# Kernel optimization log

Hardware: AMD Instinct MI355X
Metric: run time of the kernel (lower is better)

The kernel has to match this reference:

```python
import jax, jax.numpy as jnp
import numpy as np

NUM_CLASSES = 20
NUM_ANCHORS = 3
BBOX_ATTRS = 5 + NUM_CLASSES
IMG_H = IMG_W = 416
IN_H = IN_W = 52
CONF_THRES = 0.5
NMS_THRES = 0.4
TOP_K = 2048


def setup_inputs() -> dict:
    key = jax.random.key(0)
    k1, _ = jax.random.split(key)
    inp = jax.random.normal(k1, (16, NUM_ANCHORS * BBOX_ATTRS, IN_H, IN_W), dtype=jnp.float32)
    anchors = jnp.array([[116.0, 90.0], [156.0, 198.0], [373.0, 326.0]], dtype=jnp.float32)
    return {"input": inp, "anchors": anchors}


def decode(inp, anchors):
    """YOLOv3 head decode (YOLOv3Loss.forward with targets=None).
    inp: [B, A*(5+C), H, W] -> output: [B, A*H*W, 5+C] with (cx, cy, w, h, conf, cls...)."""
    bs = inp.shape[0]
    stride_h = IMG_H / IN_H
    stride_w = IMG_W / IN_W
    scaled_anchors = anchors / jnp.array([stride_w, stride_h], dtype=inp.dtype)  # [A, 2]
    # [B, A, H, W, 5+C]
    pred = inp.reshape(bs, NUM_ANCHORS, BBOX_ATTRS, IN_H, IN_W).transpose(0, 1, 3, 4, 2)
    x = jax.nn.sigmoid(pred[..., 0])
    y = jax.nn.sigmoid(pred[..., 1])
    w = pred[..., 2]
    h = pred[..., 3]
    conf = jax.nn.sigmoid(pred[..., 4])
    pred_cls = jax.nn.sigmoid(pred[..., 5:])
    grid_x = jnp.arange(IN_W, dtype=inp.dtype)[None, None, None, :]
    grid_y = jnp.arange(IN_H, dtype=inp.dtype)[None, None, :, None]
    anchor_w = scaled_anchors[:, 0][None, :, None, None]
    anchor_h = scaled_anchors[:, 1][None, :, None, None]
    bx = (x + grid_x) * stride_w
    by = (y + grid_y) * stride_h
    bw = jnp.exp(w) * anchor_w * stride_w
    bh = jnp.exp(h) * anchor_h * stride_h
    boxes = jnp.stack([bx, by, bw, bh], axis=-1).reshape(bs, -1, 4)
    output = jnp.concatenate(
        [boxes, conf.reshape(bs, -1, 1), pred_cls.reshape(bs, -1, NUM_CLASSES)], axis=-1
    )
    return output


def _nms_one(corners, conf, cls_pred):
    """Greedy class-aware NMS over TOP_K conf-sorted candidates.
    corners: [K,4] x1y1x2y2, conf: [K] desc-sorted, cls_pred: [K] int32.
    Returns keep mask [K] bool."""
    x1, y1, x2, y2 = corners[:, 0], corners[:, 1], corners[:, 2], corners[:, 3]
    area = (x2 - x1 + 1.0) * (y2 - y1 + 1.0)
    ix1 = jnp.maximum(x1[:, None], x1[None, :])
    iy1 = jnp.maximum(y1[:, None], y1[None, :])
    ix2 = jnp.minimum(x2[:, None], x2[None, :])
    iy2 = jnp.minimum(y2[:, None], y2[None, :])
    inter = jnp.clip(ix2 - ix1 + 1.0, 0.0) * jnp.clip(iy2 - iy1 + 1.0, 0.0)
    iou = inter / (area[:, None] + area[None, :] - inter + 1e-16)
    # suppress j if kept i (earlier, higher conf, same class) overlaps >= thres
    cond = (iou >= NMS_THRES) & (cls_pred[:, None] == cls_pred[None, :])
    valid = conf >= CONF_THRES
    K = conf.shape[0]
    idx = jnp.arange(K)

    def body(i, carry):
        keep, supp = carry
        ki = valid[i] & (~supp[i])
        keep = keep.at[i].set(ki)
        supp = supp | (cond[i] & (idx > i) & ki)
        return keep, supp

    keep, _ = jax.lax.fori_loop(0, K, body, (jnp.zeros(K, bool), jnp.zeros(K, bool)))
    return keep


def reference(input, anchors):
    output = decode(input, anchors)  # [B, N, 5+C]
    conf = output[..., 4]
    # top-K candidates by objectness (desc order == conf sort in original NMS)
    top_conf, top_idx = jax.lax.top_k(conf, TOP_K)  # [B, K]
    boxes = output[..., :4]
    cx, cy, w, h = boxes[..., 0], boxes[..., 1], boxes[..., 2], boxes[..., 3]
    corners = jnp.stack([cx - w / 2, cy - h / 2, cx + w / 2, cy + h / 2], axis=-1)
    corners_s = jnp.take_along_axis(corners, top_idx[..., None], axis=1)  # [B, K, 4]
    cls_pred = jnp.argmax(output[..., 5:], axis=-1).astype(jnp.int32)  # [B, N]
    cls_s = jnp.take_along_axis(cls_pred, top_idx, axis=1)  # [B, K]
    keep = jax.vmap(_nms_one)(corners_s, top_conf, cls_s)  # [B, K] bool
    return output, top_idx, keep
```

## Files before the change

### kernel.cpp

```cpp
#include <hip/hip_runtime.h>

#pragma clang fp contract(off)

#define B 16
#define A 3
#define HGT 52
#define WID 52
#define HW 2704
#define NCAND 8112
#define CATTR 25
#define TOPK 2048
#define NWORD 64
#define CH 256
#define NCHUNK (TOPK / CH)
#define GPC (CH / 32)
#define CHP 260
#define EPT 8

typedef unsigned int uint32;
typedef unsigned long long u64;

__global__ __launch_bounds__(256) void decode_kernel(const float* __restrict__ inp,
                                                     const float* __restrict__ anchors,
                                                     float* __restrict__ out,
                                                     float* __restrict__ cws,
                                                     float* __restrict__ pk) {
    __shared__ float sm[256 * CATTR];
    int tid = threadIdx.x;
    int t = blockIdx.x * 256 + tid;
    int b  = t / NCAND;
    int n  = t - b * NCAND;
    int a  = n / HW;
    int hw = n - a * HW;
    int gy = hw / WID;
    int gx = hw - gy * WID;
    const float* ip = inp + ((size_t)(b * (A * CATTR) + a * CATTR)) * HW + hw;
    float* sp = sm + tid * CATTR;

    float p0 = ip[0 * HW], p1 = ip[1 * HW], p2 = ip[2 * HW], p3 = ip[3 * HW], p4 = ip[4 * HW];
    float sx = 1.0f / (1.0f + expf(-p0));
    float sy = 1.0f / (1.0f + expf(-p1));
    float bx = (sx + (float)gx) * 8.0f;
    float by = (sy + (float)gy) * 8.0f;
    float bw = expf(p2) * anchors[a * 2 + 0];
    float bh = expf(p3) * anchors[a * 2 + 1];
    float cf = 1.0f / (1.0f + expf(-p4));
    sp[0] = bx; sp[1] = by; sp[2] = bw; sp[3] = bh; sp[4] = cf;
    cws[t] = cf;

    float best = -1.0f; int bc = 0;
#pragma unroll
    for (int c = 0; c < 20; ++c) {
        float v = ip[(5 + c) * HW];
        float s = 1.0f / (1.0f + expf(-v));
        sp[5 + c] = s;
        if (s > best) { best = s; bc = c; }
    }

    float hw_ = bw * 0.5f, hh_ = bh * 0.5f;
    float x1 = bx - hw_, y1 = by - hh_, x2 = bx + hw_, y2 = by + hh_;
    float area = ((x2 - x1) + 1.0f) * ((y2 - y1) + 1.0f);
    float4* pk4 = (float4*)(pk + (size_t)t * 8);
    pk4[0] = make_float4(x1, y1, x2, y2);
    pk4[1] = make_float4(area, (float)bc, (cf >= 0.5f) ? 1.0f : 0.0f, 0.0f);

    __syncthreads();
    const float4* sm4 = (const float4*)sm;
    float4* o4 = (float4*)(out + (size_t)blockIdx.x * 256 * CATTR);
#pragma unroll
    for (int k = 0; k < 6; ++k) o4[k * 256 + tid] = sm4[k * 256 + tid];
    if (tid < 64) o4[1536 + tid] = sm4[1536 + tid];
}

__device__ __forceinline__ void cexd(u64& a, u64& b, bool up) {
    if ((a > b) == up) { u64 tmp = a; a = b; b = tmp; }
}

__device__ __forceinline__ u64 sel(u64 k, u64 o, bool kmin) {
    return kmin ? (k < o ? k : o) : (k > o ? k : o);
}

__device__ __forceinline__ void bitonic_merge_2048(u64 key[EPT], u64* mb, int t) {
    for (unsigned j = 1024; j >= 8; j >>= 1) {
        unsigned m = j >> 3;
        bool kmin = ((t & m) == 0);
        if (m >= 64) {
            __syncthreads();
#pragma unroll
            for (int e = 0; e < EPT; ++e) mb[e * 256 + t] = key[e];
            __syncthreads();
            int pt = t ^ (int)m;
#pragma unroll
            for (int e = 0; e < EPT; ++e) key[e] = sel(key[e], mb[e * 256 + pt], kmin);
        } else {
#pragma unroll
            for (int e = 0; e < EPT; ++e) {
                u64 o = __shfl_xor(key[e], (int)m);
                key[e] = sel(key[e], o, kmin);
            }
        }
    }
    cexd(key[0], key[4], true); cexd(key[1], key[5], true);
    cexd(key[2], key[6], true); cexd(key[3], key[7], true);
    cexd(key[0], key[2], true); cexd(key[1], key[3], true);
    cexd(key[4], key[6], true); cexd(key[5], key[7], true);
    cexd(key[0], key[1], true); cexd(key[2], key[3], true);
    cexd(key[4], key[5], true); cexd(key[6], key[7], true);
}

__global__ __launch_bounds__(256) void sort1_kernel(const float* __restrict__ conf,
                                                    u64* __restrict__ runs) {
    __shared__ u64 mb[2048];
    int blk = blockIdx.x;
    int b = blk >> 2, c = blk & 3;
    int t = threadIdx.x;
    int base = t * EPT;
    int gbase = c * 2048 + base;
    const float* cp = conf + b * NCAND;

    u64 key[EPT];
    if (gbase + EPT <= NCAND) {
        const float4* cp4 = (const float4*)(cp + gbase);
        float4 c0 = cp4[0], c1 = cp4[1];
        float cf[EPT] = {c0.x, c0.y, c0.z, c0.w, c1.x, c1.y, c1.z, c1.w};
#pragma unroll
        for (int e = 0; e < EPT; ++e) {
            unsigned bits = __float_as_uint(cf[e]) | 0x80000000u;
            key[e] = ((u64)(~bits) << 32) | (unsigned)(gbase + e);
        }
    } else {
#pragma unroll
        for (int e = 0; e < EPT; ++e) {
            int idx = gbase + e;
            if (idx < NCAND) {
                unsigned bits = __float_as_uint(cp[idx]) | 0x80000000u;
                key[e] = ((u64)(~bits) << 32) | (unsigned)idx;
            } else key[e] = ~0ull;
        }
    }

    cexd(key[0], key[1], true); cexd(key[2], key[3], false);
    cexd(key[4], key[5], true); cexd(key[6], key[7], false);

    cexd(key[0], key[2], true);  cexd(key[1], key[3], true);
    cexd(key[4], key[6], false); cexd(key[5], key[7], false);
    cexd(key[0], key[1], true);  cexd(key[2], key[3], true);
    cexd(key[4], key[5], false); cexd(key[6], key[7], false);

    bool up8 = ((t & 1) == 0);
    cexd(key[0], key[4], up8); cexd(key[1], key[5], up8);
    cexd(key[2], key[6], up8); cexd(key[3], key[7], up8);
    cexd(key[0], key[2], up8); cexd(key[1], key[3], up8);
    cexd(key[4], key[6], up8); cexd(key[5], key[7], up8);
    cexd(key[0], key[1], up8); cexd(key[2], key[3], up8);
    cexd(key[4], key[5], up8); cexd(key[6], key[7], up8);

    for (unsigned k = 16; k <= 2048; k <<= 1) {
        bool up = (((unsigned)base & k) == 0);
        for (unsigned j = k >> 1; j >= 8; j >>= 1) {
            unsigned m = j >> 3;
            bool kmin = (up == ((t & m) == 0));
            if (m >= 64) {
                __syncthreads();
#pragma unroll
                for (int e = 0; e < EPT; ++e) mb[e * 256 + t] = key[e];
                __syncthreads();
                int pt = t ^ (int)m;
#pragma unroll
                for (int e = 0; e < EPT; ++e) key[e] = sel(key[e], mb[e * 256 + pt], kmin);
            } else {
#pragma unroll
                for (int e = 0; e < EPT; ++e) {
                    u64 o = __shfl_xor(key[e], (int)m);
                    key[e] = sel(key[e], o, kmin);
                }
            }
        }
        cexd(key[0], key[4], up); cexd(key[1], key[5], up);
        cexd(key[2], key[6], up); cexd(key[3], key[7], up);
        cexd(key[0], key[2], up); cexd(key[1], key[3], up);
        cexd(key[4], key[6], up); cexd(key[5], key[7], up);
        cexd(key[0], key[1], up); cexd(key[2], key[3], up);
        cexd(key[4], key[5], up); cexd(key[6], key[7], up);
    }

    u64* R = runs + ((size_t)b * 4 + c) * 2048;
#pragma unroll
    for (int e = 0; e < EPT; ++e) R[base + e] = key[e];
}

__global__ __launch_bounds__(256) void sort23_kernel(const u64* __restrict__ runs,
                                                     float* __restrict__ topf) {
    __shared__ u64 mb[2048];
    int b = blockIdx.x;
    int t = threadIdx.x;
    int base = t * EPT;
    const u64* R0 = runs + (size_t)b * 4 * 2048;

    u64 ka[EPT], kb[EPT];
#pragma unroll
    for (int e = 0; e < EPT; ++e) {
        u64 a = R0[base + e];
        u64 o = R0[2048 + 2047 - (base + e)];
        ka[e] = a < o ? a : o;
    }
    bitonic_merge_2048(ka, mb, t);
#pragma unroll
    for (int e = 0; e < EPT; ++e) {
        u64 a = R0[2 * 2048 + base + e];
        u64 o = R0[3 * 2048 + 2047 - (base + e)];
        kb[e] = a < o ? a : o;
    }
    bitonic_merge_2048(kb, mb, t);
    __syncthreads();
#pragma unroll
    for (int e = 0; e < EPT; ++e) mb[base + e] = kb[e];
    __syncthreads();
#pragma unroll
    for (int e = 0; e < EPT; ++e) {
        u64 o = mb[2047 - (base + e)];
        ka[e] = ka[e] < o ? ka[e] : o;
    }
    bitonic_merge_2048(ka, mb, t);

#pragma unroll
    for (int e = 0; e < EPT; ++e)
        topf[(size_t)b * TOPK + base + e] = (float)(unsigned)(ka[e] & 0xFFFFFFFFu);
}

__global__ __launch_bounds__(256) void geo_kernel(const float* __restrict__ pk,
                                                  const float* __restrict__ topf,
                                                  float* __restrict__ gx1,
                                                  float* __restrict__ gy1,
                                                  float* __restrict__ gx2,
                                                  float* __restrict__ gy2,
                                                  float* __restrict__ gar,
                                                  uint32* __restrict__ gcv,
                                                  uint32* __restrict__ vwords) {
    int t = blockIdx.x * 256 + threadIdx.x;
    int b = t >> 11;
    int idx = (int)topf[t];
    const float4* p4 = (const float4*)(pk + ((size_t)b * NCAND + idx) * 8);
    float4 g0 = p4[0], g1 = p4[1];
    gx1[t] = g0.x; gy1[t] = g0.y; gx2[t] = g0.z; gy2[t] = g0.w;
    gar[t] = g1.x;
    gcv[t] = (uint32)g1.y;
    bool valid = (g1.z != 0.0f);
    unsigned long long bal = __ballot(valid);
    if ((t & 63) == 0) {
        vwords[(t >> 5) + 0] = (uint32)bal;
        vwords[(t >> 5) + 1] = (uint32)(bal >> 32);
    }
}

#define KMID (13421772.5 / 33554432.0)
__global__ __launch_bounds__(1024) void build_kernel(const float* __restrict__ gx1,
                                                     const float* __restrict__ gy1,
                                                     const float* __restrict__ gx2,
                                                     const float* __restrict__ gy2,
                                                     const float* __restrict__ gar,
                                                     const uint32* __restrict__ gcv,
                                                     uint32* __restrict__ rowmask) {
    __shared__ float  x1s[TOPK], y1s[TOPK], x2s[TOPK], y2s[TOPK];
    __shared__ uint32 clss[TOPK];
    int bt   = blockIdx.y;
    int pr   = blockIdx.x;
    int tid  = threadIdx.x;
    int lane = tid & 63;
    int wv   = tid >> 6;
    int base = bt * TOPK;
    uint32* rmT = rowmask + (size_t)base * NWORD;

    for (int j = tid; j < TOPK; j += 1024) {
        int g = base + j;
        x1s[j] = gx1[g]; y1s[j] = gy1[g]; x2s[j] = gx2[g]; y2s[j] = gy2[g];
        clss[j] = gcv[g] & 0xffu;
    }
    __syncthreads();

    int r  = (wv >> 3) ? (31 - pr) : pr;
    int i0 = r * 64 + (wv & 7) * 8;

    float rx1[8], ry1[8], rx2[8], ry2[8], rar[8];
    uint32 rcl[8];
#pragma unroll
    for (int k = 0; k < 8; ++k) {
        rx1[k] = x1s[i0 + k]; ry1[k] = y1s[i0 + k];
        rx2[k] = x2s[i0 + k]; ry2[k] = y2s[i0 + k];
        rar[k] = ((rx2[k] - rx1[k]) + 1.0f) * ((ry2[k] - ry1[k]) + 1.0f);
        rcl[k] = clss[i0 + k];
    }

    int j0 = r * 64 + lane;
    float cx1 = x1s[j0], cy1 = y1s[j0], cx2 = x2s[j0], cy2 = y2s[j0];
    uint32 cc = clss[j0];

    for (int cg = r; cg < 32; ++cg) {
        float nx1 = 0.f, ny1 = 0.f, nx2 = 0.f, ny2 = 0.f; uint32 nc = 0;
        if (cg + 1 < 32) {
            int nj = (cg + 1) * 64 + lane;
            nx1 = x1s[nj]; ny1 = y1s[nj]; nx2 = x2s[nj]; ny2 = y2s[nj];
            nc = clss[nj];
        }
        float car = ((cx2 - cx1) + 1.0f) * ((cy2 - cy1) + 1.0f);
        u64 bal[8];
#pragma unroll
        for (int k = 0; k < 8; ++k) {
            float ix1 = fmaxf(rx1[k], cx1);
            float iy1 = fmaxf(ry1[k], cy1);
            float ix2 = fminf(rx2[k], cx2);
            float iy2 = fminf(ry2[k], cy2);
            float iw = fmaxf((ix2 - ix1) + 1.0f, 0.0f);
            float ih = fmaxf((iy2 - iy1) + 1.0f, 0.0f);
            float inter = iw * ih;
            float denom = ((rar[k] + car) - inter) + 1e-16f;
            bool cond = ((double)inter > KMID * (double)denom) && (cc == rcl[k]);
            bal[k] = __ballot(cond);
        }
        u64 v = bal[0];
#pragma unroll
        for (int k = 1; k < 8; ++k) if ((lane & 7) == k) v = bal[k];
        uint32 w32 = (lane & 8) ? (uint32)(v >> 32) : (uint32)v;
        int gi = i0 + (lane & 7);
        int wd = 2 * cg + ((lane >> 3) & 1);
        if (wd == (gi >> 5)) w32 &= ~((2u << (gi & 31)) - 1u);
        if (lane < 16) rmT[(size_t)wd * TOPK + gi] = w32;
        cx1 = nx1; cy1 = ny1; cx2 = nx2; cy2 = ny2; cc = nc;
    }
}

__device__ __forceinline__ void copy_chunk_dma(const uint32* __restrict__ rmT,
                                               uint32* dstL, int c, int wvm1, int lane) {
    int wmin = 8 * c;
    for (int w = wmin + wvm1; w < 64; w += 15) {
        const uint32* gp = rmT + (size_t)w * TOPK + c * CH + lane * 4;
        uint32* lp = dstL + w * CHP;
        __builtin_amdgcn_global_load_lds((const __attribute__((address_space(1))) void*)gp,
                                         (__attribute__((address_space(3))) void*)lp,
                                         16, 0, 0);
    }
}

__global__ __launch_bounds__(1024) void scan_kernel(const uint32* __restrict__ rowmask,
                                                    const uint32* __restrict__ vwords,
                                                    float* __restrict__ keepf) {
    __shared__ uint32 buf[2][64 * CHP];
    int bt  = blockIdx.x;
    int tid = threadIdx.x;
    int wv  = tid >> 6;
    int l   = tid & 63;
    const uint32* rmT = rowmask + (size_t)bt * TOPK * NWORD;

    uint32 supp = 0, keepw = 0;
    if (wv == 0) supp = ~vwords[bt * 64 + l];

    if (wv > 0) copy_chunk_dma(rmT, buf[0], 0, wv - 1, l);
    __syncthreads();

    for (int c = 0; c < NCHUNK; ++c) {
        if (wv > 0) {
            if (c + 1 < NCHUNK) copy_chunk_dma(rmT, buf[(c + 1) & 1], c + 1, wv - 1, l);
        } else {
            const uint32* bp = buf[c & 1];
            uint4 sq[8];
            {
                int g0 = c * GPC;
                const uint4* sp = (const uint4*)(bp + g0 * CHP);
#pragma unroll
                for (int q = 0; q < 8; ++q) sq[q] = sp[q];
            }
            for (int gl = 0; gl < GPC; ++gl) {
                int g = c * GPC + gl;
                uint4 rwq[8];
                const uint4* rp = (const uint4*)(bp + l * CHP + gl * 32);
#pragma unroll
                for (int q = 0; q < 8; ++q) rwq[q] = rp[q];
                uint32 cur = __builtin_amdgcn_readlane(supp, g);
#pragma unroll
                for (int q = 0; q < 8; ++q) {
                    uint32 s0 = sq[q].x, s1 = sq[q].y, s2 = sq[q].z, s3 = sq[q].w;
                    int k = q * 4;
                    cur |= s0 & ((((cur >> (k + 0)) & 1u)) - 1u);
                    cur |= s1 & ((((cur >> (k + 1)) & 1u)) - 1u);
                    cur |= s2 & ((((cur >> (k + 2)) & 1u)) - 1u);
                    cur |= s3 & ((((cur >> (k + 3)) & 1u)) - 1u);
                }
                uint32 keep = ~cur;
                if (l == g) keepw = keep;
                if (gl + 1 < GPC) {
                    const uint4* sp = (const uint4*)(bp + (g + 1) * CHP + (gl + 1) * 32);
#pragma unroll
                    for (int q = 0; q < 8; ++q) sq[q] = sp[q];
                }
                uint32 upd = 0;
#pragma unroll
                for (int q = 0; q < 8; ++q) {
                    int k = q * 4;
                    upd |= rwq[q].x & (uint32)(((int)(keep << (31 - (k + 0)))) >> 31);
                    upd |= rwq[q].y & (uint32)(((int)(keep << (31 - (k + 1)))) >> 31);
                    upd |= rwq[q].z & (uint32)(((int)(keep << (31 - (k + 2)))) >> 31);
                    upd |= rwq[q].w & (uint32)(((int)(keep << (31 - (k + 3)))) >> 31);
                }
                supp |= upd;
            }
        }
        __syncthreads();
    }

    if (wv == 0) {
#pragma unroll
        for (int k = 0; k < 32; ++k)
            keepf[bt * TOPK + l * 32 + k] = (float)((keepw >> k) & 1u);
    }
}

extern "C" void kernel_launch(void* const* d_in, const int* in_sizes, int n_in,
                              void* d_out, int out_size, void* d_ws, size_t ws_size,
                              hipStream_t stream) {
    const float* inp     = (const float*)d_in[0];
    const float* anchors = (const float*)d_in[1];
    float* out   = (float*)d_out;
    float* topf  = out  + (size_t)B * NCAND * CATTR;
    float* keepf = topf + (size_t)B * TOPK;

    float*  cws = (float*)d_ws;
    float*  pk  = cws + B * NCAND;
    float*  gx1 = pk  + (size_t)B * NCAND * 8;
    float*  gy1 = gx1 + B * TOPK;
    float*  gx2 = gy1 + B * TOPK;
    float*  gy2 = gx2 + B * TOPK;
    float*  gar = gy2 + B * TOPK;
    uint32* gcv = (uint32*)(gar + B * TOPK);
    uint32* rowmask = gcv + B * TOPK;
    uint32* vwords  = rowmask + (size_t)B * TOPK * NWORD;
    u64* runs = (u64*)rowmask;

    decode_kernel<<<(B * NCAND) / 256, 256, 0, stream>>>(inp, anchors, out, cws, pk);
    sort1_kernel<<<B * 4, 256, 0, stream>>>(cws, runs);
    sort23_kernel<<<B, 256, 0, stream>>>(runs, topf);
    geo_kernel<<<(B * TOPK) / 256, 256, 0, stream>>>(pk, topf, gx1, gy1, gx2, gy2, gar, gcv, vwords);
    build_kernel<<<dim3(16, B), 1024, 0, stream>>>(gx1, gy1, gx2, gy2, gar, gcv, rowmask);
    scan_kernel<<<B, 1024, 0, stream>>>(rowmask, vwords, keepf);
}
```

Baseline: 175.6 us.

## Replace single-block bitonic top-K merge with parallel merge-path rank kernels

```diff
diff --git a/kernel.cpp b/kernel.cpp
--- a/kernel.cpp
+++ b/kernel.cpp
@@ -80,34 +80,6 @@
     return kmin ? (k < o ? k : o) : (k > o ? k : o);
 }
 
-__device__ __forceinline__ void bitonic_merge_2048(u64 key[EPT], u64* mb, int t) {
-    for (unsigned j = 1024; j >= 8; j >>= 1) {
-        unsigned m = j >> 3;
-        bool kmin = ((t & m) == 0);
-        if (m >= 64) {
-            __syncthreads();
-#pragma unroll
-            for (int e = 0; e < EPT; ++e) mb[e * 256 + t] = key[e];
-            __syncthreads();
-            int pt = t ^ (int)m;
-#pragma unroll
-            for (int e = 0; e < EPT; ++e) key[e] = sel(key[e], mb[e * 256 + pt], kmin);
-        } else {
-#pragma unroll
-            for (int e = 0; e < EPT; ++e) {
-                u64 o = __shfl_xor(key[e], (int)m);
-                key[e] = sel(key[e], o, kmin);
-            }
-        }
-    }
-    cexd(key[0], key[4], true); cexd(key[1], key[5], true);
-    cexd(key[2], key[6], true); cexd(key[3], key[7], true);
-    cexd(key[0], key[2], true); cexd(key[1], key[3], true);
-    cexd(key[4], key[6], true); cexd(key[5], key[7], true);
-    cexd(key[0], key[1], true); cexd(key[2], key[3], true);
-    cexd(key[4], key[5], true); cexd(key[6], key[7], true);
-}
-
 __global__ __launch_bounds__(256) void sort1_kernel(const float* __restrict__ conf,
                                                     u64* __restrict__ runs) {
     __shared__ u64 mb[2048];
@@ -189,43 +161,36 @@
     for (int e = 0; e < EPT; ++e) R[base + e] = key[e];
 }
 
-__global__ __launch_bounds__(256) void sort23_kernel(const u64* __restrict__ runs,
+__device__ __forceinline__ u64 merge_rank(const u64* __restrict__ Aa,
+                                          const u64* __restrict__ Bb, int r) {
+    int lo = 0, hi = r;
+    while (lo < hi) {
+        int mid = (lo + hi) >> 1;
+        if (Aa[mid] < Bb[r - 1 - mid]) lo = mid + 1; else hi = mid;
+    }
+    u64 av = Aa[lo], bv = Bb[r - lo];
+    return av < bv ? av : bv;
+}
+
+__global__ __launch_bounds__(256) void merge1_kernel(const u64* __restrict__ runs,
+                                                     u64* __restrict__ mruns) {
+    int t  = blockIdx.x * 256 + threadIdx.x;
+    int bp = t >> 11;
+    int r  = t & 2047;
+    const u64* Aa = runs + (size_t)bp * 4096;
+    const u64* Bb = Aa + 2048;
+    mruns[(size_t)bp * 2048 + r] = merge_rank(Aa, Bb, r);
+}
+
+__global__ __launch_bounds__(256) void merge2_kernel(const u64* __restrict__ mruns,
                                                      float* __restrict__ topf) {
-    __shared__ u64 mb[2048];
-    int b = blockIdx.x;
-    int t = threadIdx.x;
-    int base = t * EPT;
-    const u64* R0 = runs + (size_t)b * 4 * 2048;
-
-    u64 ka[EPT], kb[EPT];
-#pragma unroll
-    for (int e = 0; e < EPT; ++e) {
-        u64 a = R0[base + e];
-        u64 o = R0[2048 + 2047 - (base + e)];
-        ka[e] = a < o ? a : o;
-    }
-    bitonic_merge_2048(ka, mb, t);
-#pragma unroll
-    for (int e = 0; e < EPT; ++e) {
-        u64 a = R0[2 * 2048 + base + e];
-        u64 o = R0[3 * 2048 + 2047 - (base + e)];
-        kb[e] = a < o ? a : o;
-    }
-    bitonic_merge_2048(kb, mb, t);
-    __syncthreads();
-#pragma unroll
-    for (int e = 0; e < EPT; ++e) mb[base + e] = kb[e];
-    __syncthreads();
-#pragma unroll
-    for (int e = 0; e < EPT; ++e) {
-        u64 o = mb[2047 - (base + e)];
-        ka[e] = ka[e] < o ? ka[e] : o;
-    }
-    bitonic_merge_2048(ka, mb, t);
-
-#pragma unroll
-    for (int e = 0; e < EPT; ++e)
-        topf[(size_t)b * TOPK + base + e] = (float)(unsigned)(ka[e] & 0xFFFFFFFFu);
+    int t = blockIdx.x * 256 + threadIdx.x;
+    int b = t >> 11;
+    int r = t & 2047;
+    const u64* Aa = mruns + (size_t)b * 4096;
+    const u64* Bb = Aa + 2048;
+    u64 key = merge_rank(Aa, Bb, r);
+    topf[t] = (float)(unsigned)(key & 0xFFFFFFFFu);
 }
 
 __global__ __launch_bounds__(256) void geo_kernel(const float* __restrict__ pk,
@@ -433,11 +398,13 @@
     uint32* gcv = (uint32*)(gar + B * TOPK);
     uint32* rowmask = gcv + B * TOPK;
     uint32* vwords  = rowmask + (size_t)B * TOPK * NWORD;
-    u64* runs = (u64*)rowmask;
+    u64* runs  = (u64*)rowmask;
+    u64* mruns = runs + (size_t)B * 4 * 2048;
 
     decode_kernel<<<(B * NCAND) / 256, 256, 0, stream>>>(inp, anchors, out, cws, pk);
     sort1_kernel<<<B * 4, 256, 0, stream>>>(cws, runs);
-    sort23_kernel<<<B, 256, 0, stream>>>(runs, topf);
+    merge1_kernel<<<(B * 2 * TOPK) / 256, 256, 0, stream>>>(runs, mruns);
+    merge2_kernel<<<(B * TOPK) / 256, 256, 0, stream>>>(mruns, topf);
     geo_kernel<<<(B * TOPK) / 256, 256, 0, stream>>>(pk, topf, gx1, gy1, gx2, gy2, gar, gcv, vwords);
     build_kernel<<<dim3(16, B), 1024, 0, stream>>>(gx1, gy1, gx2, gy2, gar, gcv, rowmask);
     scan_kernel<<<B, 1024, 0, stream>>>(rowmask, vwords, keepf);
```

Result: faster. 170.0 us (-3.2%).
